# Optimization experiments

Measured on AMD Instinct MI355X. Metric: run time of the kernel, lower is better.

## Reference

```python
import jax, jax.numpy as jnp
import numpy as np

B, C, H, W = 8, 256, 96, 96
CQ = C // 8

def conv1x1(x, w, b):
    # x: (B,C,H,W), w: (O,C), b: (O,)
    return jnp.einsum('bchw,oc->bohw', x, w) + b[None, :, None, None]

def axial_attend(q, k, v):
    # q,k: (B,CQ,H,W); v: (B,C,H,W). Criss-cross attention with masked diagonal
    # on the column (H) branch and joint softmax over H+W logits.
    Hn = q.shape[2]
    e_h = jnp.einsum('bchw,bcgw->bhwg', q, k)            # (B,H,W,H), g = h'
    eye = jnp.eye(Hn, dtype=bool)
    e_h = jnp.where(eye[None, :, None, :], -jnp.inf, e_h)  # mask h'==h (self on column)
    e_w = jnp.einsum('bchw,bchv->bhwv', q, k)            # (B,H,W,W), v = w'
    attn = jax.nn.softmax(jnp.concatenate([e_h, e_w], axis=-1), axis=-1)
    a_h, a_w = attn[..., :Hn], attn[..., Hn:]
    out_h = jnp.einsum('bcgw,bhwg->bchw', v, a_h)
    out_w = jnp.einsum('bchv,bhwv->bchw', v, a_w)
    return out_h + out_w

def setup_inputs() -> dict:
    key = jax.random.key(0)
    ks = jax.random.split(key, 16)
    s = lambda k, shape, scale=1.0: (jax.random.normal(k, shape, dtype=jnp.float32) * scale)
    return {
        'x0': s(ks[0], (B, C, H, W)),
        'x1': s(ks[1], (B, C, H, W)),
        'wq0': s(ks[2], (CQ, C), 0.06), 'bq0': s(ks[3], (CQ,), 0.06),
        'wk0': s(ks[4], (CQ, C), 0.06), 'bk0': s(ks[5], (CQ,), 0.06),
        'wv0': s(ks[6], (C, C), 0.06),  'bv0': s(ks[7], (C,), 0.06),
        'wq1': s(ks[8], (CQ, C), 0.06), 'bq1': s(ks[9], (CQ,), 0.06),
        'wk1': s(ks[10], (CQ, C), 0.06), 'bk1': s(ks[11], (CQ,), 0.06),
        'wv1': s(ks[12], (C, C), 0.06),  'bv1': s(ks[13], (C,), 0.06),
        'gamma': s(ks[14], (1,)),
    }

def reference(x0, x1, wq0, bq0, wk0, bk0, wv0, bv0, wq1, bq1, wk1, bk1, wv1, bv1, gamma):
    q0 = conv1x1(x0, wq0, bq0); k0 = conv1x1(x0, wk0, bk0); v0 = conv1x1(x0, wv0, bv0)
    q1 = conv1x1(x1, wq1, bq1); k1 = conv1x1(x1, wk1, bk1); v1 = conv1x1(x1, wv1, bv1)
    g = gamma[0]
    # stream 0 output: queries from stream 1, keys/values from stream 0
    cat0 = g * axial_attend(q1, k0, v0) + x0
    # stream 1 output: queries from stream 0, keys/values from stream 1
    cat1 = g * axial_attend(q0, k1, v1) + x1
    return (cat0, cat1)
```

## Files before the change

kernel.cpp:

```cpp
#include <hip/hip_runtime.h>
#include <hip/hip_bf16.h>


#define Bn 8
#define Cn 256
#define NHW 9216
#define PT_BS ((size_t)NHW * 64)

typedef unsigned short u16;
typedef __attribute__((ext_vector_type(8))) _Float16 f16x8;
typedef __attribute__((ext_vector_type(4))) float f32x4;

__device__ __forceinline__ float h2f(u16 v) {
  _Float16 h;
  __builtin_memcpy(&h, &v, 2);
  return (float)h;
}
__device__ __forceinline__ u16 f2h(float f) {
  _Float16 h = (_Float16)f;
  u16 v;
  __builtin_memcpy(&v, &h, 2);
  return v;
}

__global__ __launch_bounds__(256) void pack_all(const float* __restrict__ wq0, const float* __restrict__ bq0,
                                                const float* __restrict__ wk0, const float* __restrict__ bk0,
                                                const float* __restrict__ wv0, const float* __restrict__ bv0,
                                                const float* __restrict__ wq1, const float* __restrict__ bq1,
                                                const float* __restrict__ wk1, const float* __restrict__ bk1,
                                                const float* __restrict__ wv1, const float* __restrict__ bv1,
                                                u16* __restrict__ Wall0, float* __restrict__ ball0,
                                                u16* __restrict__ Wall1, float* __restrict__ ball1) {
  const int pr = blockIdx.y;
  const float* wq = pr ? wq1 : wq0;
  const float* bq = pr ? bq1 : bq0;
  const float* wk = pr ? wk1 : wk0;
  const float* bk = pr ? bk1 : bk0;
  const float* wv = pr ? wv1 : wv0;
  const float* bv = pr ? bv1 : bv0;
  u16* Wall = pr ? Wall1 : Wall0;
  float* ball = pr ? ball1 : ball0;
  int i = blockIdx.x * 256 + threadIdx.x;
  if (i < 320 * 256) {
    int o = i >> 8, c = i & 255;
    float v = (o < 32) ? wq[o * 256 + c] : (o < 64) ? wk[(o - 32) * 256 + c] : wv[(o - 64) * 256 + c];
    Wall[i] = f2h(v);
  }
  if (i < 320) ball[i] = (i < 32) ? bq[i] : (i < 64) ? bk[i - 32] : bv[i - 64];
}

__global__ __launch_bounds__(512, 4) void proj_all(const float* __restrict__ X0, const float* __restrict__ X1,
                                                   const u16* __restrict__ Wall0, const u16* __restrict__ Wall1,
                                                   const float* __restrict__ ball0, const float* __restrict__ ball1,
                                                   u16* __restrict__ Pt0, u16* __restrict__ Pt1,
                                                   u16* __restrict__ vW0, u16* __restrict__ vW1) {
  __shared__ __align__(16) u16 xs[96 * 264];
  u16* sO = xs;
  const int h = blockIdx.x, b = blockIdx.y, pr = blockIdx.z;
  const float* X = pr ? X1 : X0;
  const u16* Wall = pr ? Wall1 : Wall0;
  const float* ball = pr ? ball1 : ball0;
  u16* Pt = pr ? Pt1 : Pt0;
  u16* vW = pr ? vW1 : vW0;
  const int tid = threadIdx.x;
  const float* Xb = X + (size_t)b * Cn * NHW + h * 96;
  for (int idx = tid; idx < 1536; idx += 512) {
    int cq = idx / 24, n4 = idx % 24;
    const float* src = Xb + (size_t)(4 * cq) * NHW + n4 * 4;
    float4 v0 = *(const float4*)(src);
    float4 v1 = *(const float4*)(src + NHW);
    float4 v2 = *(const float4*)(src + 2 * NHW);
    float4 v3 = *(const float4*)(src + 3 * NHW);
    u16 c0[4] = {f2h(v0.x), f2h(v0.y), f2h(v0.z), f2h(v0.w)};
    u16 c1[4] = {f2h(v1.x), f2h(v1.y), f2h(v1.z), f2h(v1.w)};
    u16 c2[4] = {f2h(v2.x), f2h(v2.y), f2h(v2.z), f2h(v2.w)};
    u16 c3[4] = {f2h(v3.x), f2h(v3.y), f2h(v3.z), f2h(v3.w)};
    int colb = (4 * cq) ^ ((n4 & 7) << 3);
#pragma unroll
    for (int j = 0; j < 4; ++j) {
      ushort4 wv4;
      wv4.x = c0[j]; wv4.y = c1[j]; wv4.z = c2[j]; wv4.w = c3[j];
      *(ushort4*)&xs[(4 * n4 + j) * 264 + colb] = wv4;
    }
  }
  __syncthreads();
  const int lane = tid & 63, wv = tid >> 6;
  const int mg = wv >> 1, ng = wv & 1;
  const int arow = lane & 15;
  const int g = lane >> 4;
  const int kc = g * 8;
  int rbase[3], rsw[3];
#pragma unroll
  for (int nt = 0; nt < 3; ++nt) {
    int row = ng * 48 + nt * 16 + arow;
    rbase[nt] = row * 264;
    rsw[nt] = ((row >> 2) & 7) << 3;
  }
  f32x4 acc[5][3] = {};
#pragma unroll
  for (int kk = 0; kk < 8; ++kk) {
    f16x8 a5[5], b3[3];
#pragma unroll
    for (int j = 0; j < 5; ++j)
      a5[j] = *(const f16x8*)(Wall + (size_t)((mg + 4 * j) * 16 + arow) * 256 + kk * 32 + kc);
#pragma unroll
    for (int nt = 0; nt < 3; ++nt)
      b3[nt] = *(const f16x8*)&xs[rbase[nt] + ((kk * 32 + kc) ^ rsw[nt])];
#pragma unroll
    for (int j = 0; j < 5; ++j)
#pragma unroll
      for (int nt = 0; nt < 3; ++nt)
        acc[j][nt] = __builtin_amdgcn_mfma_f32_16x16x32_f16(a5[j], b3[nt], acc[j][nt], 0, 0, 0);
  }
  {
    u16* Ptb = Pt + (size_t)b * PT_BS;
    float4 bv = *(const float4*)(ball + mg * 16 + (g << 2));
#pragma unroll
    for (int nt = 0; nt < 3; ++nt) {
      int n = h * 96 + ng * 48 + nt * 16 + arow;
      f32x4 a = acc[0][nt];
      ushort4 r;
      r.x = f2h(a[0] + bv.x); r.y = f2h(a[1] + bv.y);
      r.z = f2h(a[2] + bv.z); r.w = f2h(a[3] + bv.w);
      *(ushort4*)&Ptb[(size_t)n * 64 + mg * 16 + (g << 2)] = r;
    }
  }
  __syncthreads();
  for (int r = 0; r < 2; ++r) {
#pragma unroll
    for (int jj = 0; jj < 2; ++jj) {
      int j = 2 * r + 1 + jj;
      int vt = mg + 8 * r + 4 * jj;
      float4 bv = *(const float4*)(ball + 64 + vt * 16 + (g << 2));
      float ba[4] = {bv.x, bv.y, bv.z, bv.w};
      int lrow0 = (mg + 4 * jj) * 16 + (g << 2);
#pragma unroll
      for (int nt = 0; nt < 3; ++nt) {
        int col = ng * 48 + nt * 16 + arow;
#pragma unroll
        for (int rr = 0; rr < 4; ++rr)
          sO[(lrow0 + rr) * 104 + col] = f2h(acc[j][nt][rr] + ba[rr]);
      }
    }
    __syncthreads();
    for (int idx = tid; idx < 1536; idx += 512) {
      int cc = idx / 12, c4 = idx % 12;
      *(float4*)(vW + ((size_t)(b * 96 + h) * 256 + r * 128 + cc) * 96 + c4 * 8) =
          *(const float4*)&sO[cc * 104 + c4 * 8];
    }
    __syncthreads();
  }
}

__global__ __launch_bounds__(256) void vtrans(const u16* __restrict__ vW0, const u16* __restrict__ vW1,
                                              u16* __restrict__ vH0, u16* __restrict__ vH1) {
  __shared__ u16 t[96][98];
  const int c = blockIdx.x, b = blockIdx.y;
  const u16* vWp = blockIdx.z ? vW1 : vW0;
  u16* vHp = blockIdx.z ? vH1 : vH0;
  for (int idx = threadIdx.x; idx < 4608; idx += 256) {
    int hh = idx / 48, w2 = idx % 48;
    *(unsigned int*)&t[hh][w2 * 2] =
        *(const unsigned int*)(vWp + (size_t)(b * 96 + hh) * 24576 + c * 96 + w2 * 2);
  }
  __syncthreads();
  for (int idx = threadIdx.x; idx < 4608; idx += 256) {
    int ww = idx / 48, g2 = idx % 48;
    unsigned int lo = t[g2 * 2][ww];
    unsigned int hi = t[g2 * 2 + 1][ww];
    *(unsigned int*)(vHp + (size_t)(b * 96 + ww) * 24576 + c * 96 + g2 * 2) = lo | (hi << 16);
  }
}

__global__ __launch_bounds__(384, 3) void attn_fused(const u16* __restrict__ Pt0, const u16* __restrict__ Pt1,
                                                     const u16* __restrict__ vW0, const u16* __restrict__ vH0,
                                                     const u16* __restrict__ vW1, const u16* __restrict__ vH1,
                                                     float* __restrict__ mWs, float* __restrict__ sWs,
                                                     float* __restrict__ mHs, float* __restrict__ sHs,
                                                     u16* __restrict__ tmpW0, u16* __restrict__ tmpH0,
                                                     u16* __restrict__ tmpW1, u16* __restrict__ tmpH1) {
  __shared__ __align__(16) char smem[46592];
  u16* vbuf = (u16*)smem;
  u16* qs = (u16*)smem;
  u16* ks = (u16*)(smem + 7680);
  u16* probs = (u16*)(smem + 26624);
  const int p = blockIdx.x, b = blockIdx.y, z = blockIdx.z;
  const int pass = z & 1, pair = z >> 1;
  const u16* Qpt = pair ? Pt0 : Pt1;
  const u16* Kpt = pair ? Pt1 : Pt0;
  const u16* Vp = pair ? (pass ? vH1 : vW1) : (pass ? vH0 : vW0);
  u16* tOut = pair ? (pass ? tmpH1 : tmpW1) : (pass ? tmpH0 : tmpW0);
  float* mOut = (pass ? mHs : mWs) + (size_t)pair * (Bn * 9216);
  float* sOut = (pass ? sHs : sWs) + (size_t)pair * (Bn * 9216);
  const int tid = threadIdx.x;
  const size_t nbase = (size_t)b * PT_BS;
  const size_t rowoff = pass ? (size_t)p * 64 : (size_t)p * 6144;
  const int rstride = pass ? 6144 : 64;
  for (int idx = tid; idx < 768; idx += 384) {
    int i = idx >> 3, c8 = idx & 7;
    const u16* src = (c8 < 4)
        ? Qpt + nbase + rowoff + (size_t)i * rstride + c8 * 8
        : Kpt + nbase + rowoff + (size_t)i * rstride + 32 + (c8 - 4) * 8;
    float4 v = *(const float4*)src;
    u16* dst = (c8 < 4) ? &qs[i * 40 + c8 * 8] : &ks[i * 40 + (c8 - 4) * 8];
    *(float4*)dst = v;
  }
  __syncthreads();
  const int lane = tid & 63, wv = tid >> 6;
  const int cl = lane & 15, g = lane >> 4;
  const int kc = g * 8;
  const int w0 = wv * 16;
  f32x4 eacc[6];
  {
    f16x8 aq = *(const f16x8*)&qs[(w0 + cl) * 40 + kc];
#pragma unroll
    for (int nt = 0; nt < 6; ++nt) {
      f16x8 bk = *(const f16x8*)&ks[(nt * 16 + cl) * 40 + kc];
      f32x4 zz = {0.f, 0.f, 0.f, 0.f};
      eacc[nt] = __builtin_amdgcn_mfma_f32_16x16x32_f16(aq, bk, zz, 0, 0, 0);
    }
  }
#pragma unroll
  for (int r = 0; r < 4; ++r) {
    int i = w0 + 4 * g + r;
    float m = -1e30f;
#pragma unroll
    for (int nt = 0; nt < 6; ++nt) {
      float e = eacc[nt][r];
      if (pass && (nt * 16 + cl) == i) { e = -1e30f; eacc[nt][r] = e; }
      m = fmaxf(m, e);
    }
    m = fmaxf(m, __shfl_xor(m, 1));
    m = fmaxf(m, __shfl_xor(m, 2));
    m = fmaxf(m, __shfl_xor(m, 4));
    m = fmaxf(m, __shfl_xor(m, 8));
    float s = 0.f;
#pragma unroll
    for (int nt = 0; nt < 6; ++nt) {
      float pv = __expf(eacc[nt][r] - m);
      eacc[nt][r] = pv;
      s += pv;
    }
    s += __shfl_xor(s, 1);
    s += __shfl_xor(s, 2);
    s += __shfl_xor(s, 4);
    s += __shfl_xor(s, 8);
#pragma unroll
    for (int nt = 0; nt < 6; ++nt)
      probs[i * 104 + nt * 16 + cl] = f2h(eacc[nt][r]);
    if (cl == 0) {
      size_t sidx = pass ? ((size_t)(b * 96 + i) * 96 + p) : ((size_t)(b * 96 + p) * 96 + i);
      mOut[sidx] = m;
      sOut[sidx] = s;
    }
  }
  __syncthreads();
  f16x8 af[3];
#pragma unroll
  for (int kt = 0; kt < 3; ++kt)
    af[kt] = *(const f16x8*)&probs[(w0 + cl) * 104 + kt * 32 + kc];
  const size_t vbase = (size_t)(b * 96 + p) * 24576;
  for (int half = 0; half < 2; ++half) {
    for (int idx = tid; idx < 1536; idx += 384) {
      int r = idx / 12, c4 = idx % 12;
      *(float4*)&vbuf[r * 104 + c4 * 8] =
          *(const float4*)(Vp + vbase + (size_t)(half * 128 + r) * 96 + c4 * 8);
    }
    __syncthreads();
    f32x4 acc[8];
#pragma unroll
    for (int nt = 0; nt < 8; ++nt) {
      f32x4 a = {0.f, 0.f, 0.f, 0.f};
#pragma unroll
      for (int kt = 0; kt < 3; ++kt) {
        f16x8 bf = *(const f16x8*)&vbuf[(nt * 16 + cl) * 104 + kt * 32 + kc];
        a = __builtin_amdgcn_mfma_f32_16x16x32_f16(af[kt], bf, a, 0, 0, 0);
      }
      acc[nt] = a;
    }
    __syncthreads();
#pragma unroll
    for (int nt = 0; nt < 8; ++nt) {
      int c2 = nt * 16 + cl;
      int wr = w0 + (g << 2);
#pragma unroll
      for (int r = 0; r < 4; ++r) vbuf[c2 * 104 + wr + r] = f2h(acc[nt][r]);
    }
    __syncthreads();
    for (int idx = tid; idx < 1536; idx += 384) {
      int r = idx / 12, c4 = idx % 12;
      *(float4*)(tOut + vbase + (size_t)(half * 128 + r) * 96 + c4 * 8) =
          *(const float4*)&vbuf[r * 104 + c4 * 8];
    }
    __syncthreads();
  }
}

__global__ __launch_bounds__(256) void scl_k(const float* __restrict__ mH, const float* __restrict__ sH,
                                             const float* __restrict__ mW, const float* __restrict__ sW,
                                             const float* __restrict__ gammaP, float* __restrict__ sclH,
                                             float* __restrict__ sclW) {
  int i = blockIdx.x * 256 + threadIdx.x;
  if (i >= 2 * Bn * 9216) return;
  float mh = mH[i], mw = mW[i];
  float m = fmaxf(mh, mw);
  float eh = __expf(mh - m), ew = __expf(mw - m);
  float s = sH[i] * eh + sW[i] * ew;
  float g = gammaP[0] / s;
  sclH[i] = g * eh;
  sclW[i] = g * ew;
}

__global__ __launch_bounds__(256) void tkomb(const u16* __restrict__ tmpH0, const u16* __restrict__ tmpW0,
                                             const u16* __restrict__ tmpH1, const u16* __restrict__ tmpW1,
                                             const float* __restrict__ x0, const float* __restrict__ x1,
                                             const float* __restrict__ sclH, const float* __restrict__ sclW,
                                             float* __restrict__ out) {
  __shared__ u16 t[96][108];
  const int c = blockIdx.x, b = blockIdx.y, pr = blockIdx.z;
  const u16* tmpH = pr ? tmpH1 : tmpH0;
  const u16* tmpW = pr ? tmpW1 : tmpW0;
  const float* x = pr ? x1 : x0;
  const float* sH = sclH + (size_t)pr * (Bn * 9216);
  const float* sW = sclW + (size_t)pr * (Bn * 9216);
  float* o = out + (size_t)pr * Bn * Cn * NHW;
  const int tid = threadIdx.x;
  for (int idx = tid; idx < 2304; idx += 256) {
    int w_ = idx / 24, h4 = idx % 24;
    *(ushort4*)&t[w_][h4 * 4] =
        *(const ushort4*)(tmpH + ((size_t)(b * 96 + w_) * 256 + c) * 96 + h4 * 4);
  }
  __syncthreads();
  for (int idx = tid; idx < 2304; idx += 256) {
    int h_ = idx / 24, w4 = idx % 24;
    size_t go = ((size_t)(b * 256 + c) * 96 + h_) * 96 + w4 * 4;
    float4 xv = *(const float4*)(x + go);
    ushort4 wvv = *(const ushort4*)(tmpW + ((size_t)(b * 96 + h_) * 256 + c) * 96 + w4 * 4);
    float4 sh4 = *(const float4*)(sH + (size_t)(b * 96 + h_) * 96 + w4 * 4);
    float4 sw4 = *(const float4*)(sW + (size_t)(b * 96 + h_) * 96 + w4 * 4);
    float4 ov;
    ov.x = xv.x + h2f(t[w4 * 4 + 0][h_]) * sh4.x + h2f(wvv.x) * sw4.x;
    ov.y = xv.y + h2f(t[w4 * 4 + 1][h_]) * sh4.y + h2f(wvv.y) * sw4.y;
    ov.z = xv.z + h2f(t[w4 * 4 + 2][h_]) * sh4.z + h2f(wvv.z) * sw4.z;
    ov.w = xv.w + h2f(t[w4 * 4 + 3][h_]) * sh4.w + h2f(wvv.w) * sw4.w;
    *(float4*)(o + go) = ov;
  }
}

extern "C" void kernel_launch(void* const* d_in, const int* in_sizes, int n_in,
                              void* d_out, int out_size, void* d_ws, size_t ws_size,
                              hipStream_t stream) {
  const float* x0 = (const float*)d_in[0];
  const float* x1 = (const float*)d_in[1];
  const float* wq0 = (const float*)d_in[2];
  const float* bq0 = (const float*)d_in[3];
  const float* wk0 = (const float*)d_in[4];
  const float* bk0 = (const float*)d_in[5];
  const float* wv0 = (const float*)d_in[6];
  const float* bv0 = (const float*)d_in[7];
  const float* wq1 = (const float*)d_in[8];
  const float* bq1 = (const float*)d_in[9];
  const float* wk1 = (const float*)d_in[10];
  const float* bk1 = (const float*)d_in[11];
  const float* wv1 = (const float*)d_in[12];
  const float* bv1 = (const float*)d_in[13];
  const float* gamma = (const float*)d_in[14];
  float* out = (float*)d_out;

  char* ws = (char*)d_ws;
  size_t off = 0;
  auto alloc = [&](size_t bytes) -> void* {
    void* ptr = ws + off;
    off += (bytes + 255) & ~(size_t)255;
    return ptr;
  };
  const size_t SZ_P = (size_t)Bn * NHW * 64 * 2;
  const size_t SZ_V = (size_t)Bn * NHW * Cn * 2;
  const size_t SZ_S = (size_t)Bn * 9216 * 4;
  u16* Pt0 = (u16*)alloc(SZ_P);
  u16* Pt1 = (u16*)alloc(SZ_P);
  u16* vW0 = (u16*)alloc(SZ_V);
  u16* vW1 = (u16*)alloc(SZ_V);
  u16* vH0 = (u16*)alloc(SZ_V);
  u16* vH1 = (u16*)alloc(SZ_V);
  u16* tmpW0 = (u16*)alloc(SZ_V);
  u16* tmpH0 = (u16*)alloc(SZ_V);
  u16* tmpW1 = (u16*)alloc(SZ_V);
  u16* tmpH1 = (u16*)alloc(SZ_V);
  u16* Wall0 = (u16*)alloc(320 * 256 * 2);
  u16* Wall1 = (u16*)alloc(320 * 256 * 2);
  float* ball0 = (float*)alloc(320 * 4);
  float* ball1 = (float*)alloc(320 * 4);
  float* mH = (float*)alloc(2 * SZ_S);
  float* sH = (float*)alloc(2 * SZ_S);
  float* mW = (float*)alloc(2 * SZ_S);
  float* sW = (float*)alloc(2 * SZ_S);
  float* sclH = (float*)alloc(2 * SZ_S);
  float* sclW = (float*)alloc(2 * SZ_S);
  (void)ws_size; (void)in_sizes; (void)n_in; (void)out_size;

  dim3 gpk(320, 2), gp(96, Bn, 2), gt(256, Bn, 2), ga(96, Bn, 4), gc(256, Bn, 2);
  pack_all<<<gpk, 256, 0, stream>>>(wq0, bq0, wk0, bk0, wv0, bv0,
                                    wq1, bq1, wk1, bk1, wv1, bv1,
                                    Wall0, ball0, Wall1, ball1);
  proj_all<<<gp, 512, 0, stream>>>(x0, x1, Wall0, Wall1, ball0, ball1, Pt0, Pt1, vW0, vW1);
  vtrans<<<gt, 256, 0, stream>>>(vW0, vW1, vH0, vH1);
  attn_fused<<<ga, 384, 0, stream>>>(Pt0, Pt1, vW0, vH0, vW1, vH1,
                                     mW, sW, mH, sH, tmpW0, tmpH0, tmpW1, tmpH1);
  scl_k<<<576, 256, 0, stream>>>(mH, sH, mW, sW, gamma, sclH, sclW);
  tkomb<<<gc, 256, 0, stream>>>(tmpH0, tmpW0, tmpH1, tmpW1, x0, x1, sclH, sclW, out);
}
```

Before: 317.6 us.

## Pipeline X tile loads with MFMA in projection by channel quarters

```diff
diff --git a/kernel.cpp b/kernel.cpp
--- a/kernel.cpp
+++ b/kernel.cpp
@@ -64,31 +64,17 @@
   u16* vW = pr ? vW1 : vW0;
   const int tid = threadIdx.x;
   const float* Xb = X + (size_t)b * Cn * NHW + h * 96;
-  for (int idx = tid; idx < 1536; idx += 512) {
-    int cq = idx / 24, n4 = idx % 24;
-    const float* src = Xb + (size_t)(4 * cq) * NHW + n4 * 4;
-    float4 v0 = *(const float4*)(src);
-    float4 v1 = *(const float4*)(src + NHW);
-    float4 v2 = *(const float4*)(src + 2 * NHW);
-    float4 v3 = *(const float4*)(src + 3 * NHW);
-    u16 c0[4] = {f2h(v0.x), f2h(v0.y), f2h(v0.z), f2h(v0.w)};
-    u16 c1[4] = {f2h(v1.x), f2h(v1.y), f2h(v1.z), f2h(v1.w)};
-    u16 c2[4] = {f2h(v2.x), f2h(v2.y), f2h(v2.z), f2h(v2.w)};
-    u16 c3[4] = {f2h(v3.x), f2h(v3.y), f2h(v3.z), f2h(v3.w)};
-    int colb = (4 * cq) ^ ((n4 & 7) << 3);
-#pragma unroll
-    for (int j = 0; j < 4; ++j) {
-      ushort4 wv4;
-      wv4.x = c0[j]; wv4.y = c1[j]; wv4.z = c2[j]; wv4.w = c3[j];
-      *(ushort4*)&xs[(4 * n4 + j) * 264 + colb] = wv4;
-    }
-  }
-  __syncthreads();
+  const int tcq = tid / 24, tn4 = tid % 24;
+  const bool act = tid < 384;
   const int lane = tid & 63, wv = tid >> 6;
   const int mg = wv >> 1, ng = wv & 1;
   const int arow = lane & 15;
   const int g = lane >> 4;
   const int kc = g * 8;
+  const u16* wrow[5];
+#pragma unroll
+  for (int j = 0; j < 5; ++j)
+    wrow[j] = Wall + (size_t)((mg + 4 * j) * 16 + arow) * 256 + kc;
   int rbase[3], rsw[3];
 #pragma unroll
   for (int nt = 0; nt < 3; ++nt) {
@@ -96,21 +82,60 @@
     rbase[nt] = row * 264;
     rsw[nt] = ((row >> 2) & 7) << 3;
   }
+  float4 pre[4];
+  if (act) {
+    const float* src = Xb + (size_t)(4 * tcq) * NHW + tn4 * 4;
+#pragma unroll
+    for (int j = 0; j < 4; ++j) pre[j] = *(const float4*)(src + (size_t)j * NHW);
+    int colb = (4 * tcq) ^ ((tn4 & 7) << 3);
+#pragma unroll
+    for (int i = 0; i < 4; ++i) {
+      ushort4 wv4;
+      wv4.x = f2h(((const float*)&pre[0])[i]);
+      wv4.y = f2h(((const float*)&pre[1])[i]);
+      wv4.z = f2h(((const float*)&pre[2])[i]);
+      wv4.w = f2h(((const float*)&pre[3])[i]);
+      *(ushort4*)&xs[(4 * tn4 + i) * 264 + colb] = wv4;
+    }
+  }
+  __syncthreads();
   f32x4 acc[5][3] = {};
 #pragma unroll
-  for (int kk = 0; kk < 8; ++kk) {
-    f16x8 a5[5], b3[3];
-#pragma unroll
-    for (int j = 0; j < 5; ++j)
-      a5[j] = *(const f16x8*)(Wall + (size_t)((mg + 4 * j) * 16 + arow) * 256 + kk * 32 + kc);
-#pragma unroll
-    for (int nt = 0; nt < 3; ++nt)
-      b3[nt] = *(const f16x8*)&xs[rbase[nt] + ((kk * 32 + kc) ^ rsw[nt])];
-#pragma unroll
-    for (int j = 0; j < 5; ++j)
+  for (int q = 0; q < 4; ++q) {
+    if (q < 3 && act) {
+      const float* src = Xb + (size_t)((q + 1) * 64 + 4 * tcq) * NHW + tn4 * 4;
+#pragma unroll
+      for (int j = 0; j < 4; ++j) pre[j] = *(const float4*)(src + (size_t)j * NHW);
+    }
+#pragma unroll
+    for (int kk = 2 * q; kk < 2 * q + 2; ++kk) {
+      f16x8 a5[5], b3[3];
+#pragma unroll
+      for (int j = 0; j < 5; ++j) a5[j] = *(const f16x8*)(wrow[j] + kk * 32);
 #pragma unroll
       for (int nt = 0; nt < 3; ++nt)
-        acc[j][nt] = __builtin_amdgcn_mfma_f32_16x16x32_f16(a5[j], b3[nt], acc[j][nt], 0, 0, 0);
+        b3[nt] = *(const f16x8*)&xs[rbase[nt] + ((kk * 32 + kc) ^ rsw[nt])];
+#pragma unroll
+      for (int j = 0; j < 5; ++j)
+#pragma unroll
+        for (int nt = 0; nt < 3; ++nt)
+          acc[j][nt] = __builtin_amdgcn_mfma_f32_16x16x32_f16(a5[j], b3[nt], acc[j][nt], 0, 0, 0);
+    }
+    if (q < 3) {
+      if (act) {
+        int colb = ((q + 1) * 64 + 4 * tcq) ^ ((tn4 & 7) << 3);
+#pragma unroll
+        for (int i = 0; i < 4; ++i) {
+          ushort4 wv4;
+          wv4.x = f2h(((const float*)&pre[0])[i]);
+          wv4.y = f2h(((const float*)&pre[1])[i]);
+          wv4.z = f2h(((const float*)&pre[2])[i]);
+          wv4.w = f2h(((const float*)&pre[3])[i]);
+          *(ushort4*)&xs[(4 * tn4 + i) * 264 + colb] = wv4;
+        }
+      }
+      __syncthreads();
+    }
   }
   {
     u16* Ptb = Pt + (size_t)b * PT_BS;
```

Measured after the change: 320.3 us. No clear change (+0.9%).
